# Performance work log

Measured on AMD Instinct MI355X. Metric: run time of the kernel, lower is better.

Reference implementation:

```python
import jax, jax.numpy as jnp
import numpy as np

NUM_FIELDS = 24
OP = "circular_convolution"  # or "circular_correlation"

# upper-triangular (i<j) field pair indices, matching torch.triu_indices(F, F, offset=1)
_I, _J = np.triu_indices(NUM_FIELDS, k=1)
_IDX0 = jnp.asarray(_I, dtype=jnp.int32)  # [P], P = F*(F-1)/2 = 276
_IDX1 = jnp.asarray(_J, dtype=jnp.int32)


def setup_inputs() -> dict:
    key = jax.random.key(0)
    inputs = jax.random.normal(key, (2048, NUM_FIELDS, 64), dtype=jnp.float32)
    return {"inputs": inputs}


def reference(inputs):
    # inputs: [B, F, D]; gather pairwise field embeddings -> [B, P, D]
    emb0 = inputs[:, _IDX0, :]
    emb1 = inputs[:, _IDX1, :]
    fft0 = jnp.fft.fft(emb0)  # complex64, FFT along D
    fft1 = jnp.fft.fft(emb1)
    if OP == "circular_correlation":
        fft0 = jnp.conj(fft0)
    # circular convolution/correlation via frequency-domain product; real part of ifft
    return jnp.real(jnp.fft.ifft(fft0 * fft1))  # [B, P, D]
```

## Files before the change

### kernel.cpp

```cpp
#include <hip/hip_runtime.h>
#include <stdint.h>


typedef __bf16 bf16x8 __attribute__((ext_vector_type(8)));
typedef __bf16 bf16x4 __attribute__((ext_vector_type(4)));
typedef float  f32x4  __attribute__((ext_vector_type(4)));
typedef unsigned long long u64x2 __attribute__((ext_vector_type(2)));

#define NF       24
#define DIM      64
#define NPAIR    276
#define RSTRIDE  264
#define XB_OFF   (NF * RSTRIDE)
#define XB_STRIDE 72
#define LDS_BYTES (XB_OFF + 32 * XB_STRIDE * 2)

__global__ __launch_bounds__(256, 4)
void holo_fm_kernel(const float* __restrict__ in, float* __restrict__ out)
{
    __shared__ __align__(16) unsigned char lds[LDS_BYTES];
    __bf16* xb = (__bf16*)(lds + XB_OFF);

    const int tid = threadIdx.x;
    const int b   = blockIdx.x;
    const float* xin = in + (size_t)b * (NF * DIM);

    for (int e = tid; e < (32 - NF) * XB_STRIDE; e += 256)
        xb[NF * XB_STRIDE + e] = (__bf16)0.0f;

    for (int e4 = tid; e4 < (NF * DIM) / 4; e4 += 256) {
        int f = e4 >> 4;
        int m = (e4 & 15) * 4;
        f32x4 v4 = *(const f32x4*)(xin + e4 * 4);
        __bf16 v0 = (__bf16)v4.x, v1 = (__bf16)v4.y,
               v2 = (__bf16)v4.z, v3 = (__bf16)v4.w;
        bf16x4 bv = {v0, v1, v2, v3};
        *(bf16x4*)(xb + f * XB_STRIDE + m) = bv;
        __bf16* rr = (__bf16*)(lds + f * RSTRIDE);
        int u0 = (64 - m) & 63;
        rr[u0]         = v0;  rr[u0 + 64]     = v0;
        rr[63 - m]     = v1;  rr[63 - m + 64] = v1;
        rr[62 - m]     = v2;  rr[62 - m + 64] = v2;
        rr[61 - m]     = v3;  rr[61 - m + 64] = v3;
    }
    __syncthreads();

    const int lane = tid & 63;
    const int wave = tid >> 6;
    const int ln   = lane & 15;
    const int q    = lane >> 4;

    bf16x8 bfrag0[2], bfrag1[2];
    #pragma unroll
    for (int ks = 0; ks < 2; ++ks) {
        bfrag0[ks] = *(const bf16x8*)(xb + ln        * XB_STRIDE + ks * 32 + q * 8);
        bfrag1[ks] = *(const bf16x8*)(xb + (16 + ln) * XB_STRIDE + ks * 32 + q * 8);
    }

    float* gbase = out + (size_t)b * NPAIR * DIM;

    for (int i = wave; i < NF - 1; i += 4) {
        const uint64_t* ri = (const uint64_t*)(lds + i * RSTRIDE);
        const int p0 = 23 * i - (i * (i - 1)) / 2;

        bf16x8 awin[6];
        #pragma unroll
        for (int w = 0; w < 6; ++w) {
            int ob = 2 * (16 * (w + 1) + 8 * q - ln);
            int dw = ob >> 3;
            int sh = (ob & 7) * 8;
            uint64_t w0 = ri[dw], w1 = ri[dw + 1], w2 = ri[dw + 2];
            uint64_t lo = (w0 >> sh) | ((w1 << 1) << (63 - sh));
            uint64_t hi = (w1 >> sh) | ((w2 << 1) << (63 - sh));
            u64x2 t; t.x = lo; t.y = hi;
            awin[w] = __builtin_bit_cast(bf16x8, t);
        }

        #pragma unroll
        for (int jt = 0; jt < 2; ++jt) {
            if (jt == 0 && i >= 15) continue;
            const int j = 16 * jt + ln;
            const bool valid = (j > i) & (j < NF);
            float* orow = gbase + ((size_t)(p0 + j - i - 1)) * DIM + 4 * q;
            #pragma unroll
            for (int mt = 0; mt < 4; ++mt) {
                f32x4 c = {0.f, 0.f, 0.f, 0.f};
                c = __builtin_amdgcn_mfma_f32_16x16x32_bf16(
                        awin[3 - mt], jt ? bfrag1[0] : bfrag0[0], c, 0, 0, 0);
                c = __builtin_amdgcn_mfma_f32_16x16x32_bf16(
                        awin[5 - mt], jt ? bfrag1[1] : bfrag0[1], c, 0, 0, 0);
                if (valid)
                    *(f32x4*)(orow + 16 * mt) = c;
            }
        }
    }
}

extern "C" void kernel_launch(void* const* d_in, const int* in_sizes, int n_in,
                              void* d_out, int out_size, void* d_ws, size_t ws_size,
                              hipStream_t stream)
{
    const float* in  = (const float*)d_in[0];
    float*       out = (float*)d_out;
    const int batches = in_sizes[0] / (NF * DIM);
    holo_fm_kernel<<<dim3(batches), dim3(256), 0, stream>>>(in, out);
}
```

Before: 154.9 us.

## Precompute shifted circulant copies in LDS to replace per-lane funnel-shift window loads

```diff
diff --git a/kernel.cpp b/kernel.cpp
--- a/kernel.cpp
+++ b/kernel.cpp
@@ -10,16 +10,18 @@
 #define NF       24
 #define DIM      64
 #define NPAIR    276
-#define RSTRIDE  264
-#define XB_OFF   (NF * RSTRIDE)
+
 #define XB_STRIDE 72
-#define LDS_BYTES (XB_OFF + 32 * XB_STRIDE * 2)
+#define XB_BYTES  (32 * XB_STRIDE * 2)
+#define COPY_OFF  XB_BYTES
+#define FSTRIDE   1120
+#define LDS_BYTES (COPY_OFF + NF * FSTRIDE)
 
-__global__ __launch_bounds__(256, 4)
+__global__ __launch_bounds__(256, 5)
 void holo_fm_kernel(const float* __restrict__ in, float* __restrict__ out)
 {
     __shared__ __align__(16) unsigned char lds[LDS_BYTES];
-    __bf16* xb = (__bf16*)(lds + XB_OFF);
+    __bf16* xb = (__bf16*)lds;
 
     const int tid = threadIdx.x;
     const int b   = blockIdx.x;
@@ -32,18 +34,38 @@
         int f = e4 >> 4;
         int m = (e4 & 15) * 4;
         f32x4 v4 = *(const f32x4*)(xin + e4 * 4);
-        __bf16 v0 = (__bf16)v4.x, v1 = (__bf16)v4.y,
-               v2 = (__bf16)v4.z, v3 = (__bf16)v4.w;
-        bf16x4 bv = {v0, v1, v2, v3};
+        __bf16 vv0 = (__bf16)v4.x, vv1 = (__bf16)v4.y,
+               vv2 = (__bf16)v4.z, vv3 = (__bf16)v4.w;
+        bf16x4 bv = {vv0, vv1, vv2, vv3};
         *(bf16x4*)(xb + f * XB_STRIDE + m) = bv;
-        __bf16* rr = (__bf16*)(lds + f * RSTRIDE);
-        int u0 = (64 - m) & 63;
-        rr[u0]         = v0;  rr[u0 + 64]     = v0;
-        rr[63 - m]     = v1;  rr[63 - m + 64] = v1;
-        rr[62 - m]     = v2;  rr[62 - m + 64] = v2;
-        rr[61 - m]     = v3;  rr[61 - m + 64] = v3;
+        __bf16* rr = (__bf16*)(lds + COPY_OFF + f * FSTRIDE);
+        __bf16 vk[4] = {vv0, vv1, vv2, vv3};
+        #pragma unroll
+        for (int k = 0; k < 4; ++k) {
+            int u = (64 - (m + k)) & 63;
+            rr[u]      = vk[k];
+            rr[u + 64] = vk[k];
+            if (u < 4) rr[u + 128] = vk[k];
+        }
     }
     __syncthreads();
+
+    for (int t = tid; t < NF * 3 * 16; t += 256) {
+        int f  = t / 48;
+        int r  = t - f * 48;
+        int cc = (r >> 4) + 1;
+        int k  = r & 15;
+        unsigned char* fb = lds + COPY_OFF + f * FSTRIDE;
+        const uint64_t* rx = (const uint64_t*)fb;
+        uint64_t A  = rx[2 * k];
+        uint64_t B  = rx[2 * k + 1];
+        uint64_t C2 = rx[2 * k + 2];
+        int sh = cc << 4;
+        uint64_t lo = (A >> sh) | (B  << (64 - sh));
+        uint64_t hi = (B >> sh) | (C2 << (64 - sh));
+        u64x2 w2; w2.x = lo; w2.y = hi;
+        *(u64x2*)(fb + 288 * cc + 16 * k) = w2;
+    }
 
     const int lane = tid & 63;
     const int wave = tid >> 6;
@@ -56,24 +78,25 @@
         bfrag0[ks] = *(const bf16x8*)(xb + ln        * XB_STRIDE + ks * 32 + q * 8);
         bfrag1[ks] = *(const bf16x8*)(xb + (16 + ln) * XB_STRIDE + ks * 32 + q * 8);
     }
+    __syncthreads();
+
+    const int cc    = (4 - (ln & 3)) & 3;
+    const int elem0 = 16 + 8 * q - ln - cc;
+    const unsigned char* abase = lds + COPY_OFF + 288 * cc + 2 * elem0;
 
     float* gbase = out + (size_t)b * NPAIR * DIM;
 
     for (int i = wave; i < NF - 1; i += 4) {
-        const uint64_t* ri = (const uint64_t*)(lds + i * RSTRIDE);
+        const unsigned char* ap = abase + i * FSTRIDE;
         const int p0 = 23 * i - (i * (i - 1)) / 2;
 
         bf16x8 awin[6];
         #pragma unroll
         for (int w = 0; w < 6; ++w) {
-            int ob = 2 * (16 * (w + 1) + 8 * q - ln);
-            int dw = ob >> 3;
-            int sh = (ob & 7) * 8;
-            uint64_t w0 = ri[dw], w1 = ri[dw + 1], w2 = ri[dw + 2];
-            uint64_t lo = (w0 >> sh) | ((w1 << 1) << (63 - sh));
-            uint64_t hi = (w1 >> sh) | ((w2 << 1) << (63 - sh));
-            u64x2 t; t.x = lo; t.y = hi;
-            awin[w] = __builtin_bit_cast(bf16x8, t);
+            uint64_t lo = *(const uint64_t*)(ap + 32 * w);
+            uint64_t hi = *(const uint64_t*)(ap + 32 * w + 8);
+            u64x2 t2; t2.x = lo; t2.y = hi;
+            awin[w] = __builtin_bit_cast(bf16x8, t2);
         }
 
         #pragma unroll
```

Result: no change. 154.0 us (-0.6%).
